# Optimization experiments

Measured on AMD Instinct MI355X. Metric: run time of the kernel, lower is better.

Reference implementation:

```python
import jax, jax.numpy as jnp
import numpy as np

N_NODES = 100000
N_EDGES = 3200000
N_GRAPHS = 512
HID = 64
OUT = 10


def setup_inputs() -> dict:
    key = jax.random.key(0)
    ks = jax.random.split(key, 10)
    x = jax.random.normal(ks[0], (N_NODES,), dtype=jnp.float32)
    edge_index = jax.random.randint(ks[1], (2, N_EDGES), 0, N_NODES, dtype=jnp.int64)
    batch = jnp.sort(jax.random.randint(ks[2], (N_NODES,), 0, N_GRAPHS, dtype=jnp.int64))
    # GCNConv weights (glorot) and zero biases, Linear layer params
    W1 = jax.random.normal(ks[3], (1, HID), dtype=jnp.float32) * (1.0 / np.sqrt(1 + HID))
    b1 = jnp.zeros((HID,), dtype=jnp.float32)
    W2 = jax.random.normal(ks[4], (HID, HID), dtype=jnp.float32) * (1.0 / np.sqrt(2 * HID))
    b2 = jnp.zeros((HID,), dtype=jnp.float32)
    Wl = jax.random.normal(ks[5], (2 * HID, OUT), dtype=jnp.float32) * (1.0 / np.sqrt(2 * HID))
    bl = jnp.zeros((OUT,), dtype=jnp.float32)
    return {"x": x, "edge_index": edge_index, "batch": batch,
            "W1": W1, "b1": b1, "W2": W2, "b2": b2, "Wl": Wl, "bl": bl}


def reference(x, edge_index, batch, W1, b1, W2, b2, Wl, bl):
    N = x.shape[0]
    loop = jnp.arange(N, dtype=edge_index.dtype)
    src = jnp.concatenate([edge_index[0], loop])  # add self-loops
    dst = jnp.concatenate([edge_index[1], loop])
    # symmetric GCN normalization: D^{-1/2} A_hat D^{-1/2}
    deg = jax.ops.segment_sum(jnp.ones_like(dst, dtype=jnp.float32), dst, num_segments=N)
    dinv = jax.lax.rsqrt(jnp.maximum(deg, 1.0))
    norm = (dinv[src] * dinv[dst])[:, None]  # [E+N, 1]

    def gcn(h, W, b):
        m = (h @ W)[src] * norm  # transform then gather messages
        return jax.ops.segment_sum(m, dst, num_segments=N) + b

    h0 = x[:, None]  # [N, 1] (dropout is identity at eval)
    x1 = jax.nn.relu(gcn(h0, W1, b1))
    x2 = jax.nn.relu(gcn(x1, W2, b2))
    xj = jnp.concatenate([x1, x2], axis=-1)  # JK 'cat' -> [N, 128]
    # global mean pool per graph
    cnt = jax.ops.segment_sum(jnp.ones((N,), jnp.float32), batch, num_segments=N_GRAPHS)
    pooled = jax.ops.segment_sum(xj, batch, num_segments=N_GRAPHS) / jnp.maximum(cnt, 1.0)[:, None]
    return pooled @ Wl + bl  # [G, 10]
```

## Files before the change

### kernel.cpp

```cpp
#include <hip/hip_runtime.h>
#include <hip/hip_bf16.h>

#define N_NODES 100000
#define N_EDGES 3200000
#define N_GRAPHS 512
#define HID 64
#define OUT_DIM 10

#define NPB 98
#define NB  1021
#define CAP 3584

__global__ __launch_bounds__(256) void k_part(const int4* __restrict__ src4,
                                              const int4* __restrict__ dst4,
                                              unsigned* __restrict__ bcur,
                                              unsigned* __restrict__ ebuf) {
    __shared__ unsigned hist[NB];
    __shared__ unsigned curs[NB];
    int tid = threadIdx.x;
    for (int i = tid; i < NB; i += 256) hist[i] = 0;
    __syncthreads();
    int4 s[2], d[2];
    int base4 = (blockIdx.x * 256 + tid) * 2;
    #pragma unroll
    for (int k = 0; k < 2; k++) {
        int i4 = base4 + k;
        if (i4 < N_EDGES / 4) { s[k] = src4[i4]; d[k] = dst4[i4]; }
        else { s[k] = make_int4(-1, -1, -1, -1); d[k] = make_int4(0, 0, 0, 0); }
    }
    #pragma unroll
    for (int k = 0; k < 2; k++) {
        if (s[k].x >= 0) {
            atomicAdd(&hist[d[k].x / NPB], 1u);
            atomicAdd(&hist[d[k].y / NPB], 1u);
            atomicAdd(&hist[d[k].z / NPB], 1u);
            atomicAdd(&hist[d[k].w / NPB], 1u);
        }
    }
    __syncthreads();
    for (int b = tid; b < NB; b += 256) {
        unsigned c = hist[b];
        curs[b] = c ? atomicAdd(&bcur[b], c) : 0u;
    }
    __syncthreads();
    #pragma unroll
    for (int k = 0; k < 2; k++) {
        if (s[k].x >= 0) {
            int ss[4] = { s[k].x, s[k].y, s[k].z, s[k].w };
            int dd[4] = { d[k].x, d[k].y, d[k].z, d[k].w };
            #pragma unroll
            for (int m = 0; m < 4; m++) {
                int b = dd[m] / NPB;
                unsigned dl = (unsigned)(dd[m] - b * NPB);
                unsigned slot = atomicAdd(&curs[b], 1u);
                ebuf[(size_t)b * CAP + slot] = (dl << 24) | (unsigned)ss[m];
            }
        }
    }
}

__global__ __launch_bounds__(256) void k_buck1(const unsigned* __restrict__ ebuf,
                                               const unsigned* __restrict__ bcur,
                                               const float* __restrict__ x,
                                               unsigned* __restrict__ deg,
                                               float* __restrict__ dinv,
                                               float* __restrict__ g1) {
    __shared__ unsigned cnt[NPB];
    int b = blockIdx.x, tid = threadIdx.x;
    if (tid < NPB) cnt[tid] = 0;
    __syncthreads();
    int ec = (int)bcur[b];
    const unsigned* eb = ebuf + (size_t)b * CAP;
    for (int i = tid; i < ec; i += 256)
        atomicAdd(&cnt[eb[i] >> 24], 1u);
    __syncthreads();
    int n0 = b * NPB;
    int nn = min(NPB, N_NODES - n0);
    if (tid < nn) {
        unsigned c = cnt[tid];
        float dn = 1.0f / sqrtf((float)c + 1.0f);
        deg[n0 + tid] = c;
        dinv[n0 + tid] = dn;
        g1[n0 + tid] = dn * x[n0 + tid];
    }
}

__global__ __launch_bounds__(256) void k_buck2(const unsigned* __restrict__ ebuf,
                                               const unsigned* __restrict__ bcur,
                                               const float* __restrict__ g1,
                                               const float* __restrict__ dinv,
                                               const float* __restrict__ x,
                                               float2* __restrict__ sd) {
    __shared__ float sacc[NPB];
    int b = blockIdx.x, tid = threadIdx.x;
    if (tid < NPB) sacc[tid] = 0.f;
    __syncthreads();
    int ec = (int)bcur[b];
    const unsigned* eb = ebuf + (size_t)b * CAP;
    for (int i = tid; i < ec; i += 256) {
        unsigned w = eb[i];
        atomicAdd(&sacc[w >> 24], g1[w & 0x00FFFFFFu]);
    }
    __syncthreads();
    int n0 = b * NPB;
    int nn = min(NPB, N_NODES - n0);
    if (tid < nn) {
        float dn = dinv[n0 + tid];
        float s = dn * (sacc[tid] + dn * x[n0 + tid]);
        sd[n0 + tid] = make_float2(s, dn);
    }
}

__global__ __launch_bounds__(256) void k_buck3(const unsigned* __restrict__ ebuf,
                                               const unsigned* __restrict__ bcur,
                                               const unsigned* __restrict__ deg,
                                               const float2* __restrict__ sd,
                                               const int* __restrict__ batch,
                                               const float* __restrict__ W1,
                                               const float* __restrict__ b1,
                                               const float* __restrict__ W2,
                                               const float* __restrict__ b2,
                                               float* __restrict__ pooled1,
                                               float* __restrict__ pooled2) {
    __shared__ unsigned sorted[CAP];
    __shared__ float2 stage[256];
    __shared__ int offs[NPB + 1];
    __shared__ unsigned curs[NPB];
    int b = blockIdx.x, tid = threadIdx.x;
    int lane = tid & 63, wv = tid >> 6;
    int n0 = b * NPB;
    int nn = min(NPB, N_NODES - n0);
    if (tid == 0) {
        int r = 0;
        for (int i = 0; i < nn; i++) { offs[i] = r; curs[i] = (unsigned)r; r += (int)deg[n0 + i]; }
        offs[nn] = r;
    }
    float w2col[HID];
    #pragma unroll
    for (int j = 0; j < HID; j++) w2col[j] = W2[j * HID + lane];
    float w1 = W1[lane], bb1 = b1[lane], bb2 = b2[lane];
    __syncthreads();
    int ec = (int)bcur[b];
    const unsigned* eb = ebuf + (size_t)b * CAP;
    for (int i = tid; i < ec; i += 256) {
        unsigned w = eb[i];
        unsigned slot = atomicAdd(&curs[w >> 24], 1u);
        sorted[slot] = w;
    }
    __syncthreads();
    float2* st = stage + wv * 64;
    int curg = -1;
    float pacc1 = 0.f, pacc2 = 0.f;
    for (int n = wv; n < nn; n += 4) {
        int lo = offs[n], hi = offs[n + 1];
        float acca = 0.f, accb = 0.f;
        for (int base = lo; base < hi; base += 64) {
            int m = hi - base; if (m > 64) m = 64;
            float2 v = make_float2(0.f, 0.f);
            if (lane < m) v = sd[sorted[base + lane] & 0x00FFFFFFu];
            st[lane] = v;
            int k = 0;
            for (; k + 1 < m; k += 2) {
                float2 e0 = st[k];
                float2 e1 = st[k + 1];
                acca = fmaf(e0.y, fmaxf(fmaf(e0.x, w1, bb1), 0.f), acca);
                accb = fmaf(e1.y, fmaxf(fmaf(e1.x, w1, bb1), 0.f), accb);
            }
            if (k < m) {
                float2 e0 = st[k];
                acca = fmaf(e0.y, fmaxf(fmaf(e0.x, w1, bb1), 0.f), acca);
            }
        }
        float2 self = sd[n0 + n];
        float t = fmaxf(fmaf(self.x, w1, bb1), 0.f);
        float a = self.y * (acca + accb + self.y * t);
        float acc2a = bb2, acc2b = 0.f;
        #pragma unroll
        for (int j = 0; j < HID; j += 2) {
            float aj0 = __int_as_float(__builtin_amdgcn_readlane(__float_as_int(a), j));
            float aj1 = __int_as_float(__builtin_amdgcn_readlane(__float_as_int(a), j + 1));
            acc2a = fmaf(aj0, w2col[j], acc2a);
            acc2b = fmaf(aj1, w2col[j + 1], acc2b);
        }
        float x2v = fmaxf(acc2a + acc2b, 0.f);
        int g = batch[n0 + n];
        if (g != curg) {
            if (curg >= 0) {
                atomicAdd(&pooled1[curg * HID + lane], pacc1);
                atomicAdd(&pooled2[curg * HID + lane], pacc2);
            }
            curg = g; pacc1 = 0.f; pacc2 = 0.f;
        }
        pacc1 += t;
        pacc2 += x2v;
    }
    if (curg >= 0) {
        atomicAdd(&pooled1[curg * HID + lane], pacc1);
        atomicAdd(&pooled2[curg * HID + lane], pacc2);
    }
}

__global__ void k_bounds(const int* __restrict__ batch, int* __restrict__ gstart) {
    int i = blockIdx.x * blockDim.x + threadIdx.x;
    if (i >= N_NODES) return;
    int b = batch[i];
    if (i == 0) {
        for (int g = 0; g <= b; g++) gstart[g] = 0;
    } else {
        int pb = batch[i - 1];
        for (int g = pb + 1; g <= b; g++) gstart[g] = i;
    }
    if (i == N_NODES - 1) {
        for (int g = b + 1; g <= N_GRAPHS; g++) gstart[g] = N_NODES;
    }
}

__global__ __launch_bounds__(128) void k_head(const float* __restrict__ pooled1,
                                              const float* __restrict__ pooled2,
                                              const int* __restrict__ gstart,
                                              const float* __restrict__ Wl,
                                              const float* __restrict__ bl,
                                              float* __restrict__ out) {
    int g = blockIdx.x;
    int t = threadIdx.x;
    float denom = fmaxf((float)(gstart[g + 1] - gstart[g]), 1.f);
    __shared__ float pl[2 * HID];
    if (t < HID) pl[t] = pooled1[g * HID + t] / denom;
    else         pl[t] = pooled2[g * HID + (t - HID)] / denom;
    __syncthreads();
    if (t < OUT_DIM) {
        float r = bl[t];
        #pragma unroll 16
        for (int j = 0; j < 2 * HID; j++) r = fmaf(pl[j], Wl[j * OUT_DIM + t], r);
        out[g * OUT_DIM + t] = r;
    }
}

extern "C" void kernel_launch(void* const* d_in, const int* in_sizes, int n_in,
                              void* d_out, int out_size, void* d_ws, size_t ws_size,
                              hipStream_t stream) {
    const float* x      = (const float*)d_in[0];
    const int*   ei     = (const int*)d_in[1];
    const int*   batch  = (const int*)d_in[2];
    const float* W1     = (const float*)d_in[3];
    const float* b1     = (const float*)d_in[4];
    const float* W2     = (const float*)d_in[5];
    const float* b2     = (const float*)d_in[6];
    const float* Wl     = (const float*)d_in[7];
    const float* bl     = (const float*)d_in[8];
    float* out = (float*)d_out;

    const int* src = ei;
    const int* dst = ei + N_EDGES;

    char* p = (char*)d_ws;
    auto alloc = [&](size_t bytes) { void* r = (void*)p; p += (bytes + 255) & ~(size_t)255; return r; };
    unsigned* bcur    = (unsigned*)alloc(NB * 4);
    unsigned* ebuf    = (unsigned*)alloc((size_t)NB * CAP * 4);
    unsigned* deg     = (unsigned*)alloc(N_NODES * 4);
    float*    dinv    = (float*)alloc(N_NODES * 4);
    float*    g1      = (float*)alloc(N_NODES * 4);
    float2*   sd      = (float2*)alloc((size_t)N_NODES * 8);
    float*    pooled1 = (float*)alloc((size_t)N_GRAPHS * HID * 4);
    float*    pooled2 = (float*)alloc((size_t)N_GRAPHS * HID * 4);
    int*      gstart  = (int*)alloc((N_GRAPHS + 1) * 4);

    hipMemsetAsync(bcur, 0, NB * 4, stream);
    hipMemsetAsync(pooled1, 0, (size_t)N_GRAPHS * HID * 4, stream);
    hipMemsetAsync(pooled2, 0, (size_t)N_GRAPHS * HID * 4, stream);

    const int TB = 256;
    int pbl = (N_EDGES / 8 + TB - 1) / TB;
    int nbl = (N_NODES + TB - 1) / TB;

    k_part <<<pbl, TB, 0, stream>>>((const int4*)src, (const int4*)dst, bcur, ebuf);
    k_buck1<<<NB, TB, 0, stream>>>(ebuf, bcur, x, deg, dinv, g1);
    k_buck2<<<NB, TB, 0, stream>>>(ebuf, bcur, g1, dinv, x, sd);
    k_bounds<<<nbl, TB, 0, stream>>>(batch, gstart);
    k_buck3<<<NB, TB, 0, stream>>>(ebuf, bcur, deg, sd, batch, W1, b1, W2, b2, pooled1, pooled2);
    k_head <<<N_GRAPHS, 128, 0, stream>>>(pooled1, pooled2, gstart, Wl, bl, out);
}
```

Before: 257.0 us.

## Shrink buckets to 64 nodes, prefetch next node gather, drop bounds kernel

Sets the bucket size to 64 nodes so bucket index and local offset become shifts and masks, which also raises the block count and lowers the per-bucket edge capacity. In k_buck3 the first 64-neighbour gather for the next node is fetched while the current node is processed, LDS reads are widened to float4, and a min-blocks launch bound is added. The two pooled buffers are merged into one, and the k_bounds kernel is removed; k_head now finds graph sizes by binary search on batch. Smaller buckets raise the risk of overflowing the per-bucket capacity on skewed degree distributions, and the launch bound may add register pressure given the 64-entry W2 column held per thread.

```diff
diff --git a/kernel.cpp b/kernel.cpp
--- a/kernel.cpp
+++ b/kernel.cpp
@@ -7,9 +7,9 @@
 #define HID 64
 #define OUT_DIM 10
 
-#define NPB 98
-#define NB  1021
-#define CAP 3584
+#define NPB 64
+#define NB  1563
+#define CAP 2432
 
 __global__ __launch_bounds__(256) void k_part(const int4* __restrict__ src4,
                                               const int4* __restrict__ dst4,
@@ -31,10 +31,10 @@
     #pragma unroll
     for (int k = 0; k < 2; k++) {
         if (s[k].x >= 0) {
-            atomicAdd(&hist[d[k].x / NPB], 1u);
-            atomicAdd(&hist[d[k].y / NPB], 1u);
-            atomicAdd(&hist[d[k].z / NPB], 1u);
-            atomicAdd(&hist[d[k].w / NPB], 1u);
+            atomicAdd(&hist[d[k].x >> 6], 1u);
+            atomicAdd(&hist[d[k].y >> 6], 1u);
+            atomicAdd(&hist[d[k].z >> 6], 1u);
+            atomicAdd(&hist[d[k].w >> 6], 1u);
         }
     }
     __syncthreads();
@@ -50,8 +50,8 @@
             int dd[4] = { d[k].x, d[k].y, d[k].z, d[k].w };
             #pragma unroll
             for (int m = 0; m < 4; m++) {
-                int b = dd[m] / NPB;
-                unsigned dl = (unsigned)(dd[m] - b * NPB);
+                int b = dd[m] >> 6;
+                unsigned dl = (unsigned)(dd[m] & 63);
                 unsigned slot = atomicAdd(&curs[b], 1u);
                 ebuf[(size_t)b * CAP + slot] = (dl << 24) | (unsigned)ss[m];
             }
@@ -111,17 +111,16 @@
     }
 }
 
-__global__ __launch_bounds__(256) void k_buck3(const unsigned* __restrict__ ebuf,
-                                               const unsigned* __restrict__ bcur,
-                                               const unsigned* __restrict__ deg,
-                                               const float2* __restrict__ sd,
-                                               const int* __restrict__ batch,
-                                               const float* __restrict__ W1,
-                                               const float* __restrict__ b1,
-                                               const float* __restrict__ W2,
-                                               const float* __restrict__ b2,
-                                               float* __restrict__ pooled1,
-                                               float* __restrict__ pooled2) {
+__global__ __launch_bounds__(256, 4) void k_buck3(const unsigned* __restrict__ ebuf,
+                                                  const unsigned* __restrict__ bcur,
+                                                  const unsigned* __restrict__ deg,
+                                                  const float2* __restrict__ sd,
+                                                  const int* __restrict__ batch,
+                                                  const float* __restrict__ W1,
+                                                  const float* __restrict__ b1,
+                                                  const float* __restrict__ W2,
+                                                  const float* __restrict__ b2,
+                                                  float* __restrict__ pooled) {
     __shared__ unsigned sorted[CAP];
     __shared__ float2 stage[256];
     __shared__ int offs[NPB + 1];
@@ -149,25 +148,50 @@
     }
     __syncthreads();
     float2* st = stage + wv * 64;
+    const float4* stv = (const float4*)st;
     int curg = -1;
     float pacc1 = 0.f, pacc2 = 0.f;
+
+    auto fetchv = [&](int n) -> float2 {
+        float2 v = make_float2(0.f, 0.f);
+        if (n < nn) {
+            int lo = offs[n];
+            int m = offs[n + 1] - lo; if (m > 64) m = 64;
+            if (lane < m) v = sd[sorted[lo + lane] & 0x00FFFFFFu];
+        }
+        return v;
+    };
+
+    float2 vcur = fetchv(wv);
     for (int n = wv; n < nn; n += 4) {
+        float2 vnext = fetchv(n + 4);
         int lo = offs[n], hi = offs[n + 1];
+        int m = hi - lo; if (m > 64) m = 64;
+        st[lane] = vcur;
         float acca = 0.f, accb = 0.f;
-        for (int base = lo; base < hi; base += 64) {
-            int m = hi - base; if (m > 64) m = 64;
+        int k = 0;
+        for (; k + 1 < m; k += 2) {
+            float4 e = stv[k >> 1];
+            acca = fmaf(e.y, fmaxf(fmaf(e.x, w1, bb1), 0.f), acca);
+            accb = fmaf(e.w, fmaxf(fmaf(e.z, w1, bb1), 0.f), accb);
+        }
+        if (k < m) {
+            float2 e0 = st[k];
+            acca = fmaf(e0.y, fmaxf(fmaf(e0.x, w1, bb1), 0.f), acca);
+        }
+        for (int base = lo + 64; base < hi; base += 64) {
+            int mm = hi - base; if (mm > 64) mm = 64;
             float2 v = make_float2(0.f, 0.f);
-            if (lane < m) v = sd[sorted[base + lane] & 0x00FFFFFFu];
+            if (lane < mm) v = sd[sorted[base + lane] & 0x00FFFFFFu];
             st[lane] = v;
-            int k = 0;
-            for (; k + 1 < m; k += 2) {
-                float2 e0 = st[k];
-                float2 e1 = st[k + 1];
-                acca = fmaf(e0.y, fmaxf(fmaf(e0.x, w1, bb1), 0.f), acca);
-                accb = fmaf(e1.y, fmaxf(fmaf(e1.x, w1, bb1), 0.f), accb);
-            }
-            if (k < m) {
-                float2 e0 = st[k];
+            int kk = 0;
+            for (; kk + 1 < mm; kk += 2) {
+                float4 e = stv[kk >> 1];
+                acca = fmaf(e.y, fmaxf(fmaf(e.x, w1, bb1), 0.f), acca);
+                accb = fmaf(e.w, fmaxf(fmaf(e.z, w1, bb1), 0.f), accb);
+            }
+            if (kk < mm) {
+                float2 e0 = st[kk];
                 acca = fmaf(e0.y, fmaxf(fmaf(e0.x, w1, bb1), 0.f), acca);
             }
         }
@@ -186,47 +210,35 @@
         int g = batch[n0 + n];
         if (g != curg) {
             if (curg >= 0) {
-                atomicAdd(&pooled1[curg * HID + lane], pacc1);
-                atomicAdd(&pooled2[curg * HID + lane], pacc2);
+                atomicAdd(&pooled[curg * 2 * HID + lane], pacc1);
+                atomicAdd(&pooled[curg * 2 * HID + HID + lane], pacc2);
             }
             curg = g; pacc1 = 0.f; pacc2 = 0.f;
         }
         pacc1 += t;
         pacc2 += x2v;
+        vcur = vnext;
     }
     if (curg >= 0) {
-        atomicAdd(&pooled1[curg * HID + lane], pacc1);
-        atomicAdd(&pooled2[curg * HID + lane], pacc2);
-    }
-}
-
-__global__ void k_bounds(const int* __restrict__ batch, int* __restrict__ gstart) {
-    int i = blockIdx.x * blockDim.x + threadIdx.x;
-    if (i >= N_NODES) return;
-    int b = batch[i];
-    if (i == 0) {
-        for (int g = 0; g <= b; g++) gstart[g] = 0;
-    } else {
-        int pb = batch[i - 1];
-        for (int g = pb + 1; g <= b; g++) gstart[g] = i;
-    }
-    if (i == N_NODES - 1) {
-        for (int g = b + 1; g <= N_GRAPHS; g++) gstart[g] = N_NODES;
-    }
-}
-
-__global__ __launch_bounds__(128) void k_head(const float* __restrict__ pooled1,
-                                              const float* __restrict__ pooled2,
-                                              const int* __restrict__ gstart,
+        atomicAdd(&pooled[curg * 2 * HID + lane], pacc1);
+        atomicAdd(&pooled[curg * 2 * HID + HID + lane], pacc2);
+    }
+}
+
+__global__ __launch_bounds__(128) void k_head(const float* __restrict__ pooled,
+                                              const int* __restrict__ batch,
                                               const float* __restrict__ Wl,
                                               const float* __restrict__ bl,
                                               float* __restrict__ out) {
     int g = blockIdx.x;
     int t = threadIdx.x;
-    float denom = fmaxf((float)(gstart[g + 1] - gstart[g]), 1.f);
+    int lo1 = 0, hi1 = N_NODES;
+    while (lo1 < hi1) { int mid = (lo1 + hi1) >> 1; if (batch[mid] < g) lo1 = mid + 1; else hi1 = mid; }
+    int lo2 = lo1, hi2 = N_NODES;
+    while (lo2 < hi2) { int mid = (lo2 + hi2) >> 1; if (batch[mid] < g + 1) lo2 = mid + 1; else hi2 = mid; }
+    float denom = fmaxf((float)(lo2 - lo1), 1.f);
     __shared__ float pl[2 * HID];
-    if (t < HID) pl[t] = pooled1[g * HID + t] / denom;
-    else         pl[t] = pooled2[g * HID + (t - HID)] / denom;
+    pl[t] = pooled[g * 2 * HID + t] / denom;
     __syncthreads();
     if (t < OUT_DIM) {
         float r = bl[t];
@@ -255,28 +267,23 @@
 
     char* p = (char*)d_ws;
     auto alloc = [&](size_t bytes) { void* r = (void*)p; p += (bytes + 255) & ~(size_t)255; return r; };
-    unsigned* bcur    = (unsigned*)alloc(NB * 4);
-    unsigned* ebuf    = (unsigned*)alloc((size_t)NB * CAP * 4);
-    unsigned* deg     = (unsigned*)alloc(N_NODES * 4);
-    float*    dinv    = (float*)alloc(N_NODES * 4);
-    float*    g1      = (float*)alloc(N_NODES * 4);
-    float2*   sd      = (float2*)alloc((size_t)N_NODES * 8);
-    float*    pooled1 = (float*)alloc((size_t)N_GRAPHS * HID * 4);
-    float*    pooled2 = (float*)alloc((size_t)N_GRAPHS * HID * 4);
-    int*      gstart  = (int*)alloc((N_GRAPHS + 1) * 4);
+    unsigned* bcur   = (unsigned*)alloc(NB * 4);
+    unsigned* ebuf   = (unsigned*)alloc((size_t)NB * CAP * 4);
+    unsigned* deg    = (unsigned*)alloc(N_NODES * 4);
+    float*    dinv   = (float*)alloc(N_NODES * 4);
+    float*    g1     = (float*)alloc(N_NODES * 4);
+    float2*   sd     = (float2*)alloc((size_t)N_NODES * 8);
+    float*    pooled = (float*)alloc((size_t)N_GRAPHS * 2 * HID * 4);
 
     hipMemsetAsync(bcur, 0, NB * 4, stream);
-    hipMemsetAsync(pooled1, 0, (size_t)N_GRAPHS * HID * 4, stream);
-    hipMemsetAsync(pooled2, 0, (size_t)N_GRAPHS * HID * 4, stream);
+    hipMemsetAsync(pooled, 0, (size_t)N_GRAPHS * 2 * HID * 4, stream);
 
     const int TB = 256;
     int pbl = (N_EDGES / 8 + TB - 1) / TB;
-    int nbl = (N_NODES + TB - 1) / TB;
 
     k_part <<<pbl, TB, 0, stream>>>((const int4*)src, (const int4*)dst, bcur, ebuf);
     k_buck1<<<NB, TB, 0, stream>>>(ebuf, bcur, x, deg, dinv, g1);
     k_buck2<<<NB, TB, 0, stream>>>(ebuf, bcur, g1, dinv, x, sd);
-    k_bounds<<<nbl, TB, 0, stream>>>(batch, gstart);
-    k_buck3<<<NB, TB, 0, stream>>>(ebuf, bcur, deg, sd, batch, W1, b1, W2, b2, pooled1, pooled2);
-    k_head <<<N_GRAPHS, 128, 0, stream>>>(pooled1, pooled2, gstart, Wl, bl, out);
-}
+    k_buck3<<<NB, TB, 0, stream>>>(ebuf, bcur, deg, sd, batch, W1, b1, W2, b2, pooled);
+    k_head <<<N_GRAPHS, 128, 0, stream>>>(pooled, batch, Wl, bl, out);
+}
```

Result: slower. 268.9 us (+4.7%).
